# Performance work log

Hardware: AMD Instinct MI355X
Metric: run time of the kernel (lower is better)

## Reference

```python
import jax, jax.numpy as jnp
import numpy as np

N = 100000      # nodes
E = 3200000     # edges (avg degree 32)
D_IN = 128
H = 32          # hidden_dim
OUT = 8         # output_dim
EPS = 1e-5


def setup_inputs() -> dict:
    key = jax.random.key(0)
    ks = jax.random.split(key, 18)
    s = 0.05
    return {
        "x": jax.random.normal(ks[0], (N, D_IN), jnp.float32),
        "edge_index": jax.random.randint(ks[1], (2, E), 0, N, dtype=jnp.int32),
        # GCNConv weights (stored as [in, out]) and biases
        "W0": jax.random.normal(ks[2], (D_IN, H), jnp.float32) * s,
        "b0": jnp.zeros((H,), jnp.float32),
        "W1": jax.random.normal(ks[3], (H, H), jnp.float32) * s,
        "b1": jnp.zeros((H,), jnp.float32),
        "W2": jax.random.normal(ks[4], (H, H), jnp.float32) * s,
        "b2": jnp.zeros((H,), jnp.float32),
        # LayerNorms after layers 0 and 1 (num_layers-1 = 2 LNs)
        "ln0_g": jnp.ones((H,), jnp.float32),
        "ln0_b": jnp.zeros((H,), jnp.float32),
        "ln1_g": jnp.ones((H,), jnp.float32),
        "ln1_b": jnp.zeros((H,), jnp.float32),
        # post_mp: Linear(H, H//2) -> ReLU -> Linear(H//2, OUT)
        "mp_w1": jax.random.normal(ks[5], (H, H // 2), jnp.float32) * s,
        "mp_b1": jnp.zeros((H // 2,), jnp.float32),
        "mp_w2": jax.random.normal(ks[6], (H // 2, OUT), jnp.float32) * s,
        "mp_b2": jnp.zeros((OUT,), jnp.float32),
    }


def _layernorm(x, g, b):
    m = jnp.mean(x, axis=-1, keepdims=True)
    v = jnp.var(x, axis=-1, keepdims=True)
    return (x - m) * jax.lax.rsqrt(v + EPS) * g + b


def _gcn(x, W, bias, src, dst, norm):
    # GCNConv: theta(x) then normalized gather-scatter aggregation + bias
    h = x @ W                               # [N, out]
    msg = h[src] * norm[:, None]            # gather along edges
    out = jax.ops.segment_sum(msg, dst, num_segments=N)  # scatter-add
    return out + bias


def reference(x, edge_index, W0, b0, W1, b1, W2, b2,
              ln0_g, ln0_b, ln1_g, ln1_b, mp_w1, mp_b1, mp_w2, mp_b2):
    # add self-loops (PyG GCNConv default) and symmetric normalization
    loop = jnp.arange(N, dtype=edge_index.dtype)
    src = jnp.concatenate([edge_index[0], loop])
    dst = jnp.concatenate([edge_index[1], loop])
    deg = jax.ops.segment_sum(jnp.ones_like(dst, jnp.float32), dst, num_segments=N)
    dis = jnp.where(deg > 0, jax.lax.rsqrt(jnp.maximum(deg, 1.0)), 0.0)
    norm = dis[src] * dis[dst]              # [E+N]

    # dropout p=0.05 is inference-mode -> identity
    h = jax.nn.relu(_gcn(x, W0, b0, src, dst, norm))
    h = _layernorm(h, ln0_g, ln0_b)
    h = jax.nn.relu(_gcn(h, W1, b1, src, dst, norm))
    h = _layernorm(h, ln1_g, ln1_b)
    h = jax.nn.relu(_gcn(h, W2, b2, src, dst, norm))  # last layer: no LN

    # post_mp head
    h = jax.nn.relu(h @ mp_w1 + mp_b1)
    h = h @ mp_w2 + mp_b2
    return jax.nn.log_softmax(h, axis=1)
```

## Files before the change

### kernel.cpp

```cpp
#include <hip/hip_runtime.h>

#define NN 100000
#define NE 3200000
#define DIN 128
#define HD 32
#define MID 16
#define OUTD 8
#define LN_EPS 1e-5f

#define BINSHIFT 8
#define NB 391
#define CAP 10240
#define EPB 8192
#define ABS 1024
#define AITER (EPB / ABS)
#define CBS 1024

typedef float float4_v __attribute__((ext_vector_type(4)));
typedef short short8   __attribute__((ext_vector_type(8)));
typedef float f32x4    __attribute__((ext_vector_type(4)));


__device__ __forceinline__ float bf2f(unsigned short u) {
    union { unsigned int i; float f; } c;
    c.i = ((unsigned int)u) << 16;
    return c.f;
}
__device__ __forceinline__ unsigned short f2bf(float f) {
    union { float f; unsigned int i; } c;
    c.f = f;
    unsigned int r = c.i + 0x7FFFu + ((c.i >> 16) & 1u);
    return (unsigned short)(r >> 16);
}
__device__ __forceinline__ unsigned int pack2(float a, float b) {
    return (unsigned int)f2bf(a) | ((unsigned int)f2bf(b) << 16);
}
__device__ __forceinline__ void addpk(float& a0, float& a1, unsigned int u) {
    union { unsigned int i; float f; } lo, hi;
    lo.i = u << 16;
    hi.i = u & 0xFFFF0000u;
    a0 += lo.f;
    a1 += hi.f;
}


__global__ void k_zero_bins(int* __restrict__ g_bincur) {
    int i = blockIdx.x * blockDim.x + threadIdx.x;
    if (i < NB) g_bincur[i] = 0;
}

__global__ __launch_bounds__(ABS) void k_binA(const int* __restrict__ src,
                                              const int* __restrict__ dst,
                                              int* __restrict__ g_bincur,
                                              unsigned int* __restrict__ staged) {
    __shared__ int cnt[512];
    __shared__ int obin[512];
    __shared__ int base[NB];
    __shared__ unsigned short sbin[EPB];
    __shared__ unsigned int sedge[EPB];
    int tid = threadIdx.x;
    if (tid < 512) cnt[tid] = 0;
    __syncthreads();
    int e0 = blockIdx.x * EPB;
    int total = min(EPB, NE - e0);
    int dreg[AITER];
#pragma unroll
    for (int i = 0; i < AITER; ++i) {
        int e = e0 + i * ABS + tid;
        dreg[i] = (e < NE) ? dst[e] : -1;
        if (dreg[i] >= 0) atomicAdd(&cnt[dreg[i] >> BINSHIFT], 1);
    }
    __syncthreads();
    int v = 0;
    if (tid < 512) {
        v = cnt[tid];
        obin[tid] = v;
    }
    __syncthreads();
#pragma unroll
    for (int off = 1; off < 512; off <<= 1) {
        int t = (tid < 512 && tid >= off) ? obin[tid - off] : 0;
        __syncthreads();
        if (tid < 512) obin[tid] += t;
        __syncthreads();
    }
    if (tid < 512) obin[tid] -= v;
    __syncthreads();
    if (tid < NB) {
        int c = cnt[tid];
        base[tid] = c ? atomicAdd(&g_bincur[tid], c) : 0;
        int s0 = obin[tid];
        for (int k = 0; k < c; ++k) sbin[s0 + k] = (unsigned short)tid;
    }
    if (tid < 512) cnt[tid] = 0;
    __syncthreads();
#pragma unroll
    for (int i = 0; i < AITER; ++i) {
        int e = e0 + i * ABS + tid;
        int d = dreg[i];
        if (d >= 0) {
            int b = d >> BINSHIFT;
            int slot = obin[b] + atomicAdd(&cnt[b], 1);
            sedge[slot] = ((unsigned int)(d & 255) << 24) | (unsigned int)src[e];
        }
    }
    __syncthreads();
#pragma unroll
    for (int i = 0; i < AITER; ++i) {
        int s = i * ABS + tid;
        if (s < total) {
            int b = sbin[s];
            int k = base[b] + (s - obin[b]);
            if (k < CAP) staged[(size_t)b * CAP + k] = sedge[s];
        }
    }
}

__global__ void k_binscan(const int* __restrict__ g_bincur, int* __restrict__ g_binexcl,
                          int* __restrict__ row_ptr) {
    __shared__ int s[512];
    int v = (threadIdx.x < NB) ? min(g_bincur[threadIdx.x], CAP) : 0;
    s[threadIdx.x] = v;
    __syncthreads();
#pragma unroll
    for (int off = 1; off < 512; off <<= 1) {
        int t = (threadIdx.x >= off) ? s[threadIdx.x - off] : 0;
        __syncthreads();
        s[threadIdx.x] += t;
        __syncthreads();
    }
    if (threadIdx.x < NB) g_binexcl[threadIdx.x] = s[threadIdx.x] - v;
    if (threadIdx.x == NB - 1) row_ptr[NN] = s[threadIdx.x];
}

__global__ __launch_bounds__(CBS) void k_binC(const int* __restrict__ g_bincur,
                                              const int* __restrict__ g_binexcl,
                                              const unsigned int* __restrict__ staged,
                                              int* __restrict__ row_ptr,
                                              float* __restrict__ dis,
                                              int* __restrict__ csr_src) {
    __shared__ int cnt[256];
    __shared__ int scn[256];
    int b = blockIdx.x;
    int tid = threadIdx.x;
    int tot = min(g_bincur[b], CAP);
    if (tid < 256) cnt[tid] = 0;
    __syncthreads();
    const unsigned int* st = staged + (size_t)b * CAP;
    for (int i = tid; i < tot; i += CBS)
        atomicAdd(&cnt[st[i] >> 24], 1);
    __syncthreads();
    int v = 0;
    if (tid < 256) {
        v = cnt[tid];
        scn[tid] = v;
    }
    __syncthreads();
#pragma unroll
    for (int off = 1; off < 256; off <<= 1) {
        int t = (tid < 256 && tid >= off) ? scn[tid - off] : 0;
        __syncthreads();
        if (tid < 256) scn[tid] += t;
        __syncthreads();
    }
    int gbase = g_binexcl[b];
    if (tid < 256) {
        int excl = scn[tid] - v;
        int node = (b << BINSHIFT) + tid;
        if (node < NN) {
            row_ptr[node] = gbase + excl;
            dis[node] = rsqrtf((float)(v + 1));
        }
        cnt[tid] = excl;
    }
    __syncthreads();
    for (int i = tid; i < tot; i += CBS) {
        unsigned int p = st[i];
        int rank = atomicAdd(&cnt[p >> 24], 1);
        csr_src[gbase + rank] = (int)(p & 0xFFFFFFu);
    }
}


template <int K>
__global__ __launch_bounds__(256) void k_gemm_mfma(const float* __restrict__ x,
                                                   const float* __restrict__ W,
                                                   const float* __restrict__ dis,
                                                   unsigned short* __restrict__ hs) {
    constexpr int XP = K + 8;
    __shared__ unsigned short xb[64 * XP];
    __shared__ unsigned short wt[HD * XP];
    __shared__ float sdis[64];
    int tid = threadIdx.x;
    int n0 = blockIdx.x * 64;
    for (int f = tid; f < K * HD; f += 256) {
        int k = f >> 5, j = f & 31;
        wt[j * XP + k] = f2bf(W[f]);
    }
    if (tid < 64) {
        int nn = n0 + tid;
        sdis[tid] = dis[nn < NN ? nn : NN - 1];
    }
    constexpr int FQ = K / 4;
    for (int f = tid; f < 64 * FQ; f += 256) {
        int node = f / FQ, kq = f % FQ;
        int nn = n0 + node;
        if (nn < NN) {
            float4 xv = *reinterpret_cast<const float4*>(x + (size_t)nn * K + kq * 4);
            unsigned short* p = &xb[node * XP + kq * 4];
            p[0] = f2bf(xv.x);
            p[1] = f2bf(xv.y);
            p[2] = f2bf(xv.z);
            p[3] = f2bf(xv.w);
        }
    }
    __syncthreads();
    int w = tid >> 6, l = tid & 63;
    int arow = l & 15, kg = l >> 4;
    f32x4 acc0 = {0.f, 0.f, 0.f, 0.f};
    f32x4 acc1 = {0.f, 0.f, 0.f, 0.f};
#pragma unroll
    for (int ks = 0; ks < K / 32; ++ks) {
        short8 a  = *reinterpret_cast<const short8*>(&xb[(w * 16 + arow) * XP + ks * 32 + kg * 8]);
        short8 b0 = *reinterpret_cast<const short8*>(&wt[arow * XP + ks * 32 + kg * 8]);
        short8 b1 = *reinterpret_cast<const short8*>(&wt[(16 + arow) * XP + ks * 32 + kg * 8]);
        acc0 = __builtin_amdgcn_mfma_f32_16x16x32_bf16(a, b0, acc0, 0, 0, 0);
        acc1 = __builtin_amdgcn_mfma_f32_16x16x32_bf16(a, b1, acc1, 0, 0, 0);
    }
#pragma unroll
    for (int r = 0; r < 4; ++r) {
        int nloc = w * 16 + kg * 4 + r;
        int nn = n0 + nloc;
        if (nn < NN) {
            float d = sdis[nloc];
            hs[(size_t)nn * HD + arow]      = f2bf(acc0[r] * d);
            hs[(size_t)nn * HD + 16 + arow] = f2bf(acc1[r] * d);
        }
    }
}


template <int K>
__global__ __launch_bounds__(256) void k_gemm(const float* __restrict__ x,
                                              const float* __restrict__ W,
                                              const float* __restrict__ dis,
                                              unsigned short* __restrict__ hs) {
    __shared__ float sW[K * HD];
    for (int t = threadIdx.x; t < K * HD; t += 256) sW[t] = W[t];
    __syncthreads();
    int lane = threadIdx.x & 63;
    int q = __builtin_amdgcn_readfirstlane(threadIdx.x >> 6);
    int n = blockIdx.x * 64 + lane;
    if (n >= NN) return;
    const float* xr = x + (size_t)n * K;
    const float* Wq = sW + q * 8;
    float acc[8];
#pragma unroll
    for (int j = 0; j < 8; ++j) acc[j] = 0.f;
    for (int k0 = 0; k0 < K; k0 += 4) {
        float4 xv = *reinterpret_cast<const float4*>(xr + k0);
#pragma unroll
        for (int kk = 0; kk < 4; ++kk) {
            float xk = kk == 0 ? xv.x : kk == 1 ? xv.y : kk == 2 ? xv.z : xv.w;
#pragma unroll
            for (int j = 0; j < 8; ++j)
                acc[j] = fmaf(xk, Wq[(k0 + kk) * HD + j], acc[j]);
        }
    }
    float d = dis[n];
    uint4 p;
    p.x = pack2(acc[0] * d, acc[1] * d);
    p.y = pack2(acc[2] * d, acc[3] * d);
    p.z = pack2(acc[4] * d, acc[5] * d);
    p.w = pack2(acc[6] * d, acc[7] * d);
    *reinterpret_cast<uint4*>(hs + (size_t)n * HD + q * 8) = p;
}


#define G4(si) \
    { \
        uint2 g0 = *reinterpret_cast<const uint2*>(h + (size_t)(si).x * HD + c0); \
        uint2 g1 = *reinterpret_cast<const uint2*>(h + (size_t)(si).y * HD + c0); \
        uint2 g2 = *reinterpret_cast<const uint2*>(h + (size_t)(si).z * HD + c0); \
        uint2 g3 = *reinterpret_cast<const uint2*>(h + (size_t)(si).w * HD + c0); \
        addpk(a0, a1, g0.x); addpk(a2, a3, g0.y); \
        addpk(a0, a1, g1.x); addpk(a2, a3, g1.y); \
        addpk(a0, a1, g2.x); addpk(a2, a3, g2.y); \
        addpk(a0, a1, g3.x); addpk(a2, a3, g3.y); \
    }

template <int DO_LN>
__global__ __launch_bounds__(256) void k_gather(
        const int* __restrict__ row_ptr, const int* __restrict__ csr_src,
        const float* __restrict__ dis, const unsigned short* __restrict__ h,
        const float* __restrict__ bias, const float* __restrict__ g,
        const float* __restrict__ bln, float* __restrict__ out) {
    int idx = blockIdx.x * blockDim.x + threadIdx.x;
    int n = idx >> 3, sub = idx & 7;
    if (n >= NN) return;
    int c0 = sub << 2;

    uint2 u = *reinterpret_cast<const uint2*>(h + (size_t)n * HD + c0);
    float a0 = 0.f, a1 = 0.f, a2 = 0.f, a3 = 0.f;
    addpk(a0, a1, u.x);
    addpk(a2, a3, u.y);

    int e = row_ptr[n], end = row_ptr[n + 1];
    while (e < end && (e & 3)) {
        int s = csr_src[e];
        uint2 hv = *reinterpret_cast<const uint2*>(h + (size_t)s * HD + c0);
        addpk(a0, a1, hv.x);
        addpk(a2, a3, hv.y);
        ++e;
    }
    for (; e + 15 < end; e += 16) {
        int4 s0 = *reinterpret_cast<const int4*>(csr_src + e);
        int4 s1 = *reinterpret_cast<const int4*>(csr_src + e + 4);
        int4 s2 = *reinterpret_cast<const int4*>(csr_src + e + 8);
        int4 s3 = *reinterpret_cast<const int4*>(csr_src + e + 12);
        uint2 g0 = *reinterpret_cast<const uint2*>(h + (size_t)s0.x * HD + c0);
        uint2 g1 = *reinterpret_cast<const uint2*>(h + (size_t)s0.y * HD + c0);
        uint2 g2 = *reinterpret_cast<const uint2*>(h + (size_t)s0.z * HD + c0);
        uint2 g3 = *reinterpret_cast<const uint2*>(h + (size_t)s0.w * HD + c0);
        uint2 g4 = *reinterpret_cast<const uint2*>(h + (size_t)s1.x * HD + c0);
        uint2 g5 = *reinterpret_cast<const uint2*>(h + (size_t)s1.y * HD + c0);
        uint2 g6 = *reinterpret_cast<const uint2*>(h + (size_t)s1.z * HD + c0);
        uint2 g7 = *reinterpret_cast<const uint2*>(h + (size_t)s1.w * HD + c0);
        uint2 g8 = *reinterpret_cast<const uint2*>(h + (size_t)s2.x * HD + c0);
        uint2 g9 = *reinterpret_cast<const uint2*>(h + (size_t)s2.y * HD + c0);
        uint2 ga = *reinterpret_cast<const uint2*>(h + (size_t)s2.z * HD + c0);
        uint2 gb = *reinterpret_cast<const uint2*>(h + (size_t)s2.w * HD + c0);
        uint2 gc = *reinterpret_cast<const uint2*>(h + (size_t)s3.x * HD + c0);
        uint2 gd = *reinterpret_cast<const uint2*>(h + (size_t)s3.y * HD + c0);
        uint2 ge = *reinterpret_cast<const uint2*>(h + (size_t)s3.z * HD + c0);
        uint2 gf = *reinterpret_cast<const uint2*>(h + (size_t)s3.w * HD + c0);
        addpk(a0, a1, g0.x); addpk(a2, a3, g0.y);
        addpk(a0, a1, g1.x); addpk(a2, a3, g1.y);
        addpk(a0, a1, g2.x); addpk(a2, a3, g2.y);
        addpk(a0, a1, g3.x); addpk(a2, a3, g3.y);
        addpk(a0, a1, g4.x); addpk(a2, a3, g4.y);
        addpk(a0, a1, g5.x); addpk(a2, a3, g5.y);
        addpk(a0, a1, g6.x); addpk(a2, a3, g6.y);
        addpk(a0, a1, g7.x); addpk(a2, a3, g7.y);
        addpk(a0, a1, g8.x); addpk(a2, a3, g8.y);
        addpk(a0, a1, g9.x); addpk(a2, a3, g9.y);
        addpk(a0, a1, ga.x); addpk(a2, a3, ga.y);
        addpk(a0, a1, gb.x); addpk(a2, a3, gb.y);
        addpk(a0, a1, gc.x); addpk(a2, a3, gc.y);
        addpk(a0, a1, gd.x); addpk(a2, a3, gd.y);
        addpk(a0, a1, ge.x); addpk(a2, a3, ge.y);
        addpk(a0, a1, gf.x); addpk(a2, a3, gf.y);
    }
    if (e + 7 < end) {
        int4 s0 = *reinterpret_cast<const int4*>(csr_src + e);
        int4 s1 = *reinterpret_cast<const int4*>(csr_src + e + 4);
        G4(s0);
        G4(s1);
        e += 8;
    }
    if (e + 3 < end) {
        int4 s0 = *reinterpret_cast<const int4*>(csr_src + e);
        G4(s0);
        e += 4;
    }
    for (; e < end; ++e) {
        int s = csr_src[e];
        uint2 hv = *reinterpret_cast<const uint2*>(h + (size_t)s * HD + c0);
        addpk(a0, a1, hv.x);
        addpk(a2, a3, hv.y);
    }

    float d = dis[n];
    float4 bv = *reinterpret_cast<const float4*>(bias + c0);
    float v0 = fmaxf(fmaf(a0, d, bv.x), 0.f);
    float v1 = fmaxf(fmaf(a1, d, bv.y), 0.f);
    float v2 = fmaxf(fmaf(a2, d, bv.z), 0.f);
    float v3 = fmaxf(fmaf(a3, d, bv.w), 0.f);

    if (DO_LN) {
        float s = (v0 + v1) + (v2 + v3);
        float s2 = (v0 * v0 + v1 * v1) + (v2 * v2 + v3 * v3);
#pragma unroll
        for (int m = 4; m >= 1; m >>= 1) {
            s += __shfl_xor(s, m, 8);
            s2 += __shfl_xor(s2, m, 8);
        }
        float mean = s * (1.f / 32.f);
        float var = s2 * (1.f / 32.f) - mean * mean;
        float r = rsqrtf(var + LN_EPS);
        float4 gv = *reinterpret_cast<const float4*>(g + c0);
        float4 lb = *reinterpret_cast<const float4*>(bln + c0);
        v0 = (v0 - mean) * r * gv.x + lb.x;
        v1 = (v1 - mean) * r * gv.y + lb.y;
        v2 = (v2 - mean) * r * gv.z + lb.z;
        v3 = (v3 - mean) * r * gv.w + lb.w;
    }
    float4_v ov;
    ov[0] = v0; ov[1] = v1; ov[2] = v2; ov[3] = v3;
    __builtin_nontemporal_store(ov, reinterpret_cast<float4_v*>(out + (size_t)n * HD + c0));
}


__global__ void k_final(const float* __restrict__ hin,
                        const float* __restrict__ w1, const float* __restrict__ mb1,
                        const float* __restrict__ w2, const float* __restrict__ mb2,
                        float* __restrict__ out) {
    __shared__ float sw1[HD * MID], sw2[MID * OUTD], sb1[MID], sb2[OUTD];
    for (int t = threadIdx.x; t < HD * MID; t += blockDim.x) sw1[t] = w1[t];
    for (int t = threadIdx.x; t < MID * OUTD; t += blockDim.x) sw2[t] = w2[t];
    if (threadIdx.x < MID) sb1[threadIdx.x] = mb1[threadIdx.x];
    if (threadIdx.x < OUTD) sb2[threadIdx.x] = mb2[threadIdx.x];
    __syncthreads();
    int n = blockIdx.x * blockDim.x + threadIdx.x;
    if (n >= NN) return;
    float h[HD];
    const float* ar = hin + (size_t)n * HD;
#pragma unroll
    for (int k = 0; k < HD; ++k) h[k] = ar[k];
    float t[MID];
#pragma unroll
    for (int j = 0; j < MID; ++j) {
        float a = sb1[j];
#pragma unroll
        for (int k = 0; k < HD; ++k) a += h[k] * sw1[k * MID + j];
        t[j] = fmaxf(a, 0.f);
    }
    float o[OUTD];
#pragma unroll
    for (int j = 0; j < OUTD; ++j) {
        float a = sb2[j];
#pragma unroll
        for (int k = 0; k < MID; ++k) a += t[k] * sw2[k * OUTD + j];
        o[j] = a;
    }
    float mx = o[0];
#pragma unroll
    for (int j = 1; j < OUTD; ++j) mx = fmaxf(mx, o[j]);
    float se = 0.f;
#pragma unroll
    for (int j = 0; j < OUTD; ++j) se += __expf(o[j] - mx);
    float lse = __logf(se) + mx;
    float* orow = out + (size_t)n * OUTD;
#pragma unroll
    for (int j = 0; j < OUTD; ++j) orow[j] = o[j] - lse;
}


extern "C" void kernel_launch(void* const* d_in, const int* in_sizes, int n_in,
                              void* d_out, int out_size, void* d_ws, size_t ws_size,
                              hipStream_t stream) {
    const float* x     = (const float*)d_in[0];
    const int*   ei    = (const int*)d_in[1];
    const float* W0    = (const float*)d_in[2];
    const float* b0    = (const float*)d_in[3];
    const float* W1    = (const float*)d_in[4];
    const float* b1    = (const float*)d_in[5];
    const float* W2    = (const float*)d_in[6];
    const float* b2    = (const float*)d_in[7];
    const float* ln0_g = (const float*)d_in[8];
    const float* ln0_b = (const float*)d_in[9];
    const float* ln1_g = (const float*)d_in[10];
    const float* ln1_b = (const float*)d_in[11];
    const float* mp_w1 = (const float*)d_in[12];
    const float* mp_b1 = (const float*)d_in[13];
    const float* mp_w2 = (const float*)d_in[14];
    const float* mp_b2 = (const float*)d_in[15];
    float* out = (float*)d_out;

    const int* src = ei;
    const int* dst = ei + NE;

    char* w = (char*)d_ws;
    auto align256 = [](size_t v) { return (v + 255) & ~(size_t)255; };
    int* g_bincur  = (int*)w;   w += align256((size_t)NB * 4);
    int* g_binexcl = (int*)w;   w += align256((size_t)NB * 4);
    int* row_ptr   = (int*)w;   w += align256((size_t)(NN + 1) * 4);
    float* dis     = (float*)w; w += align256((size_t)NN * 4);
    char* uni = w;
    unsigned short* bufB = (unsigned short*)uni;
    float* bufA = (float*)(uni + align256((size_t)NN * HD * 2));
    unsigned int* staged = (unsigned int*)uni;
    size_t uni_sz = align256((size_t)NB * CAP * 4);
    size_t uni_sz2 = align256((size_t)NN * HD * 2) + align256((size_t)NN * HD * 4);
    w = uni + (uni_sz > uni_sz2 ? uni_sz : uni_sz2);
    int* csr_src = (int*)w;

    const int BS = 256;
    int gN  = (NN + BS - 1) / BS;
    int gA  = (NE + EPB - 1) / EPB;
    int gN8 = (NN * 8 + BS - 1) / BS;
    int gG  = (NN + 63) / 64;

    k_zero_bins<<<1, 512, 0, stream>>>(g_bincur);
    k_binA<<<gA, ABS, 0, stream>>>(src, dst, g_bincur, staged);
    k_binscan<<<1, 512, 0, stream>>>(g_bincur, g_binexcl, row_ptr);
    k_binC<<<NB, CBS, 0, stream>>>(g_bincur, g_binexcl, staged, row_ptr, dis, csr_src);

    k_gemm_mfma<DIN><<<gG, BS, 0, stream>>>(x, W0, dis, bufB);
    k_gather<1><<<gN8, BS, 0, stream>>>(row_ptr, csr_src, dis, bufB, b0,
                                        ln0_g, ln0_b, bufA);
    k_gemm<HD><<<gG, BS, 0, stream>>>(bufA, W1, dis, bufB);
    k_gather<1><<<gN8, BS, 0, stream>>>(row_ptr, csr_src, dis, bufB, b1,
                                        ln1_g, ln1_b, bufA);
    k_gemm<HD><<<gG, BS, 0, stream>>>(bufA, W2, dis, bufB);
    k_gather<0><<<gN8, BS, 0, stream>>>(row_ptr, csr_src, dis, bufB, b2,
                                        nullptr, nullptr, bufA);

    k_final<<<gN, BS, 0, stream>>>(bufA, mp_w1, mp_b1, mp_w2, mp_b2, out);
}
```

Measured before the change: 237.8 us.

## Fuse next-layer 32x32 GEMM into gather epilogue, removing separate GEMM kernels

The 32x32 dense transform for layers 1 and 2 is folded into the gather kernel's epilogue. Each node's 8-lane group shuffles its LayerNormed values and multiplies them by the weight matrix held in shared memory, then writes the bf16 pre-scaled features straight to a second ping-pong buffer. This drops two kernel launches and the fp32 intermediate write and read through global memory. In exchange, every gather block loads a 4KB weight tile and spends extra shuffles and FMAs per node, and the early return after the barrier keeps the sync safe only because it follows the weight load.

```diff
diff --git a/kernel.cpp b/kernel.cpp
--- a/kernel.cpp
+++ b/kernel.cpp
@@ -240,43 +240,6 @@
 }
 
 
-template <int K>
-__global__ __launch_bounds__(256) void k_gemm(const float* __restrict__ x,
-                                              const float* __restrict__ W,
-                                              const float* __restrict__ dis,
-                                              unsigned short* __restrict__ hs) {
-    __shared__ float sW[K * HD];
-    for (int t = threadIdx.x; t < K * HD; t += 256) sW[t] = W[t];
-    __syncthreads();
-    int lane = threadIdx.x & 63;
-    int q = __builtin_amdgcn_readfirstlane(threadIdx.x >> 6);
-    int n = blockIdx.x * 64 + lane;
-    if (n >= NN) return;
-    const float* xr = x + (size_t)n * K;
-    const float* Wq = sW + q * 8;
-    float acc[8];
-#pragma unroll
-    for (int j = 0; j < 8; ++j) acc[j] = 0.f;
-    for (int k0 = 0; k0 < K; k0 += 4) {
-        float4 xv = *reinterpret_cast<const float4*>(xr + k0);
-#pragma unroll
-        for (int kk = 0; kk < 4; ++kk) {
-            float xk = kk == 0 ? xv.x : kk == 1 ? xv.y : kk == 2 ? xv.z : xv.w;
-#pragma unroll
-            for (int j = 0; j < 8; ++j)
-                acc[j] = fmaf(xk, Wq[(k0 + kk) * HD + j], acc[j]);
-        }
-    }
-    float d = dis[n];
-    uint4 p;
-    p.x = pack2(acc[0] * d, acc[1] * d);
-    p.y = pack2(acc[2] * d, acc[3] * d);
-    p.z = pack2(acc[4] * d, acc[5] * d);
-    p.w = pack2(acc[6] * d, acc[7] * d);
-    *reinterpret_cast<uint4*>(hs + (size_t)n * HD + q * 8) = p;
-}
-
-
 #define G4(si) \
     { \
         uint2 g0 = *reinterpret_cast<const uint2*>(h + (size_t)(si).x * HD + c0); \
@@ -289,12 +252,18 @@
         addpk(a0, a1, g3.x); addpk(a2, a3, g3.y); \
     }
 
-template <int DO_LN>
+template <int DO_LN, int DO_GEMM>
 __global__ __launch_bounds__(256) void k_gather(
         const int* __restrict__ row_ptr, const int* __restrict__ csr_src,
         const float* __restrict__ dis, const unsigned short* __restrict__ h,
         const float* __restrict__ bias, const float* __restrict__ g,
-        const float* __restrict__ bln, float* __restrict__ out) {
+        const float* __restrict__ bln, const float* __restrict__ Wn,
+        float* __restrict__ outf, unsigned short* __restrict__ outh) {
+    __shared__ float sW[HD * HD];
+    if (DO_GEMM) {
+        for (int t = threadIdx.x; t < HD * HD; t += 256) sW[t] = Wn[t];
+        __syncthreads();
+    }
     int idx = blockIdx.x * blockDim.x + threadIdx.x;
     int n = idx >> 3, sub = idx & 7;
     if (n >= NN) return;
@@ -395,9 +364,33 @@
         v2 = (v2 - mean) * r * gv.z + lb.z;
         v3 = (v3 - mean) * r * gv.w + lb.w;
     }
-    float4_v ov;
-    ov[0] = v0; ov[1] = v1; ov[2] = v2; ov[3] = v3;
-    __builtin_nontemporal_store(ov, reinterpret_cast<float4_v*>(out + (size_t)n * HD + c0));
+
+    if (DO_GEMM) {
+        float y0 = 0.f, y1 = 0.f, y2 = 0.f, y3 = 0.f;
+#pragma unroll
+        for (int m = 0; m < 8; ++m) {
+            float vk0 = __shfl(v0, m, 8);
+            float vk1 = __shfl(v1, m, 8);
+            float vk2 = __shfl(v2, m, 8);
+            float vk3 = __shfl(v3, m, 8);
+            float4 w0 = *reinterpret_cast<const float4*>(&sW[(4 * m + 0) * HD + c0]);
+            float4 w1 = *reinterpret_cast<const float4*>(&sW[(4 * m + 1) * HD + c0]);
+            float4 w2 = *reinterpret_cast<const float4*>(&sW[(4 * m + 2) * HD + c0]);
+            float4 w3 = *reinterpret_cast<const float4*>(&sW[(4 * m + 3) * HD + c0]);
+            y0 = fmaf(vk0, w0.x, fmaf(vk1, w1.x, fmaf(vk2, w2.x, fmaf(vk3, w3.x, y0))));
+            y1 = fmaf(vk0, w0.y, fmaf(vk1, w1.y, fmaf(vk2, w2.y, fmaf(vk3, w3.y, y1))));
+            y2 = fmaf(vk0, w0.z, fmaf(vk1, w1.z, fmaf(vk2, w2.z, fmaf(vk3, w3.z, y2))));
+            y3 = fmaf(vk0, w0.w, fmaf(vk1, w1.w, fmaf(vk2, w2.w, fmaf(vk3, w3.w, y3))));
+        }
+        uint2 pp;
+        pp.x = pack2(y0 * d, y1 * d);
+        pp.y = pack2(y2 * d, y3 * d);
+        *reinterpret_cast<uint2*>(outh + (size_t)n * HD + c0) = pp;
+    } else {
+        float4_v ov;
+        ov[0] = v0; ov[1] = v1; ov[2] = v2; ov[3] = v3;
+        __builtin_nontemporal_store(ov, reinterpret_cast<float4_v*>(outf + (size_t)n * HD + c0));
+    }
 }
 
 
@@ -477,11 +470,13 @@
     int* row_ptr   = (int*)w;   w += align256((size_t)(NN + 1) * 4);
     float* dis     = (float*)w; w += align256((size_t)NN * 4);
     char* uni = w;
-    unsigned short* bufB = (unsigned short*)uni;
-    float* bufA = (float*)(uni + align256((size_t)NN * HD * 2));
+    size_t hs_sz = align256((size_t)NN * HD * 2);
+    unsigned short* hs0 = (unsigned short*)uni;
+    unsigned short* hs1 = (unsigned short*)(uni + hs_sz);
+    float* bufA = (float*)(uni + 2 * hs_sz);
     unsigned int* staged = (unsigned int*)uni;
     size_t uni_sz = align256((size_t)NB * CAP * 4);
-    size_t uni_sz2 = align256((size_t)NN * HD * 2) + align256((size_t)NN * HD * 4);
+    size_t uni_sz2 = 2 * hs_sz + align256((size_t)NN * HD * 4);
     w = uni + (uni_sz > uni_sz2 ? uni_sz : uni_sz2);
     int* csr_src = (int*)w;
 
@@ -496,15 +491,13 @@
     k_binscan<<<1, 512, 0, stream>>>(g_bincur, g_binexcl, row_ptr);
     k_binC<<<NB, CBS, 0, stream>>>(g_bincur, g_binexcl, staged, row_ptr, dis, csr_src);
 
-    k_gemm_mfma<DIN><<<gG, BS, 0, stream>>>(x, W0, dis, bufB);
-    k_gather<1><<<gN8, BS, 0, stream>>>(row_ptr, csr_src, dis, bufB, b0,
-                                        ln0_g, ln0_b, bufA);
-    k_gemm<HD><<<gG, BS, 0, stream>>>(bufA, W1, dis, bufB);
-    k_gather<1><<<gN8, BS, 0, stream>>>(row_ptr, csr_src, dis, bufB, b1,
-                                        ln1_g, ln1_b, bufA);
-    k_gemm<HD><<<gG, BS, 0, stream>>>(bufA, W2, dis, bufB);
-    k_gather<0><<<gN8, BS, 0, stream>>>(row_ptr, csr_src, dis, bufB, b2,
-                                        nullptr, nullptr, bufA);
+    k_gemm_mfma<DIN><<<gG, BS, 0, stream>>>(x, W0, dis, hs0);
+    k_gather<1, 1><<<gN8, BS, 0, stream>>>(row_ptr, csr_src, dis, hs0, b0,
+                                           ln0_g, ln0_b, W1, nullptr, hs1);
+    k_gather<1, 1><<<gN8, BS, 0, stream>>>(row_ptr, csr_src, dis, hs1, b1,
+                                           ln1_g, ln1_b, W2, nullptr, hs0);
+    k_gather<0, 0><<<gN8, BS, 0, stream>>>(row_ptr, csr_src, dis, hs0, b2,
+                                           nullptr, nullptr, nullptr, bufA, nullptr);
 
     k_final<<<gN, BS, 0, stream>>>(bufA, mp_w1, mp_b1, mp_w2, mp_b2, out);
 }
```

Measured after the change: 215.8 us. -9.3%, faster.
